# Kernel optimization log

Measured on AMD Instinct MI355X. Metric: run time of the kernel, lower is better.

Reference implementation:

```python
import jax, jax.numpy as jnp
import numpy as np

B_, H, N, D = 512, 8, 256, 16   # windows*batch, heads, tokens/window, head_dim
NW = 64                          # windows per image (B_ = 8 images * 64 windows)
TABLE = 961                      # (2*16-1)^2 relative position table rows
EPS = 1e-12                      # F.normalize eps


def setup_inputs() -> dict:
    key = jax.random.key(0)
    k_q, k_k, k_v, k_t, k_i, k_m = jax.random.split(key, 6)
    return {
        "q": jax.random.normal(k_q, (B_, H, N, D), dtype=jnp.float32),
        "k": jax.random.normal(k_k, (B_, H, N, D), dtype=jnp.float32),
        "v": jax.random.normal(k_v, (B_, H, N, D), dtype=jnp.float32),
        "table": jax.random.normal(k_t, (TABLE, H), dtype=jnp.float32),
        "index": jax.random.randint(k_i, (N * N,), 0, TABLE, dtype=jnp.int64),
        "mask": jax.random.normal(k_m, (NW, N, N), dtype=jnp.float32),
    }


def _l2norm(x):
    # matches F.normalize(x, dim=-1): x / max(||x||2, eps)
    n = jnp.sqrt(jnp.sum(x * x, axis=-1, keepdims=True))
    return x / jnp.maximum(n, EPS)


def reference(q, k, v, table, index, mask):
    b, h, n, d = q.shape
    # cosine-normalized QK^T: [B_, H, N, N]
    attn = jnp.einsum("bhnd,bhmd->bhnm", _l2norm(q), _l2norm(k))
    # relative position bias gather: table[index] -> (N*N, H) -> (H, N, N)
    bias = table[index].reshape(n, n, h).transpose(2, 0, 1)
    attn = attn + bias[None]
    # per-window additive mask
    nw = mask.shape[0]
    attn = attn.reshape(b // nw, nw, h, n, n) + mask[None, :, None]
    attn = attn.reshape(b, h, n, n)
    attn = jax.nn.softmax(attn, axis=-1)   # attn_drop is identity at p=0
    x = jnp.einsum("bhnm,bhmd->bhnd", attn, v)
    # transpose(1,2).reshape(B_, N, H*head_dim)
    return x.transpose(0, 2, 1, 3).reshape(b, n, h * d)
```

## Files before the change

### kernel.cpp

```cpp
#include <hip/hip_runtime.h>
#include <stdint.h>

#define HH 8
#define NN 256
#define DD 16
#define NWIN 64
#define LOG2E 1.44269504088896340736f

typedef __attribute__((ext_vector_type(8))) short short8;
typedef __attribute__((ext_vector_type(4))) short short4_t;
typedef __attribute__((ext_vector_type(4))) float f32x4;

static __device__ __forceinline__ unsigned short f2bf(float f) {
    union { float f; uint32_t u; } v; v.f = f;
    uint32_t u = v.u;
    uint32_t r = (u + 0x7fffu + ((u >> 16) & 1u)) >> 16;
    return (unsigned short)r;
}
static __device__ __forceinline__ float bf2f(uint32_t s) {
    union { uint32_t u; float f; } v; v.u = s << 16;
    return v.f;
}

__global__ void bias_perm_kernel(const float* __restrict__ table,
                                 const int* __restrict__ index,
                                 unsigned short* __restrict__ biasD) {
    int o = blockIdx.x * 256 + threadIdx.x;
    int r  = o & 3;
    int c  = (o >> 2) & 15;
    int qq = (o >> 6) & 3;
    int jt = (o >> 8) & 15;
    int it = (o >> 12) & 15;
    int h  = o >> 16;
    int i = it * 16 + c;
    int j = jt * 16 + qq * 4 + r;
    int idx = index[i * NN + j];
    biasD[o] = f2bf(table[idx * HH + h] * LOG2E);
}

__global__ void mask_perm_kernel(const float* __restrict__ mask,
                                 unsigned short* __restrict__ maskD) {
    __shared__ float lds[16 * 256];
    int w  = blockIdx.x >> 4;
    int it = blockIdx.x & 15;
    int tid = threadIdx.x;
    const float* src = mask + ((size_t)w * NN + it * 16) * NN;
    {
        int row = tid >> 4, col0 = (tid & 15) * 16;
        const float4* s4 = (const float4*)(src + row * NN + col0);
        float4* d4 = (float4*)(lds + row * 256 + col0);
        d4[0] = s4[0]; d4[1] = s4[1]; d4[2] = s4[2]; d4[3] = s4[3];
    }
    __syncthreads();
    unsigned short* dst = maskD + (size_t)blockIdx.x * 4096 + tid * 16;
    int base = tid * 16;
#pragma unroll
    for (int e = 0; e < 16; e++) {
        int o  = base + e;
        int r  = o & 3;
        int c  = (o >> 2) & 15;
        int qq = (o >> 6) & 3;
        int jt = (o >> 8) & 15;
        int j  = jt * 16 + qq * 4 + r;
        dst[e] = f2bf(lds[c * 256 + j] * LOG2E);
    }
}

__global__ __launch_bounds__(256, 2) void attn_kernel(
    const float* __restrict__ q, const float* __restrict__ k, const float* __restrict__ v,
    const unsigned short* __restrict__ biasD, const unsigned short* __restrict__ maskD,
    float* __restrict__ out)
{
    int bh = blockIdx.x;
    int b  = bh >> 3;
    int h  = bh & 7;
    int w  = b & (NWIN - 1);
    int tid  = threadIdx.x;
    int lane = tid & 63;
    int wave = tid >> 6;
    int c    = lane & 15;
    int quad = lane >> 4;

    __shared__ unsigned short Kn[256 * 20];
    __shared__ unsigned short Vl[4096];
    __shared__ float Xs[256 * 17];

    const size_t base = (size_t)bh * (NN * DD);

    {
        const float4* kr = (const float4*)(k + base + (size_t)tid * DD);
        float4 a0 = kr[0], a1 = kr[1], a2 = kr[2], a3 = kr[3];
        float x[16] = {a0.x,a0.y,a0.z,a0.w, a1.x,a1.y,a1.z,a1.w,
                       a2.x,a2.y,a2.z,a2.w, a3.x,a3.y,a3.z,a3.w};
        float ss = 0.f;
#pragma unroll
        for (int e = 0; e < 16; e++) ss += x[e] * x[e];
        float sc = 1.0f / fmaxf(sqrtf(ss), 1e-12f);
        unsigned short* dst = &Kn[tid * 20];
#pragma unroll
        for (int e = 0; e < 16; e++) dst[e] = f2bf(x[e] * sc);
    }
    {
        const float4* vr = (const float4*)(v + base + (size_t)tid * DD);
        float4 a0 = vr[0], a1 = vr[1], a2 = vr[2], a3 = vr[3];
        float x[16] = {a0.x,a0.y,a0.z,a0.w, a1.x,a1.y,a1.z,a1.w,
                       a2.x,a2.y,a2.z,a2.w, a3.x,a3.y,a3.z,a3.w};
        int j  = tid;
        int kc = j >> 5, hi = (j >> 4) & 1, qv = (j >> 2) & 3, r = j & 3;
        int jj = hi * 4 + r;
#pragma unroll
        for (int d = 0; d < 16; d++)
            Vl[((kc * 4 + qv) * 16 + d) * 8 + jj] = f2bf(x[d]);
    }
    __syncthreads();

    short8 vf[8];
#pragma unroll
    for (int kc = 0; kc < 8; kc++)
        vf[kc] = *(const short8*)&Vl[((kc * 4 + quad) * 16 + c) * 8];

    f32x4 zero = {0.f, 0.f, 0.f, 0.f};

#pragma unroll 1
    for (int t = 0; t < 4; t++) {
        int it = wave * 4 + t;
        int i0 = it * 16;

        short8 qf = {0,0,0,0,0,0,0,0};
        if (quad < 2) {
            const float4* qr = (const float4*)(q + base + (size_t)(i0 + c) * DD + quad * 8);
            float4 a0 = qr[0], a1 = qr[1];
            float x[8] = {a0.x,a0.y,a0.z,a0.w, a1.x,a1.y,a1.z,a1.w};
            float ss = 0.f;
#pragma unroll
            for (int e = 0; e < 8; e++) ss += x[e] * x[e];
            ss += __shfl_xor(ss, 16);
            float sc = LOG2E / fmaxf(sqrtf(ss), 1e-12f);
#pragma unroll
            for (int e = 0; e < 8; e++) qf[e] = (short)f2bf(x[e] * sc);
        }

        f32x4 acc[16];
#pragma unroll
        for (int jt = 0; jt < 16; jt++) {
            short8 kf = {0,0,0,0,0,0,0,0};
            if (quad < 2) {
                const unsigned short* kp = &Kn[(jt * 16 + c) * 20 + quad * 8];
                short4_t lo = *(const short4_t*)kp;
                short4_t hi = *(const short4_t*)(kp + 4);
                kf[0]=lo[0]; kf[1]=lo[1]; kf[2]=lo[2]; kf[3]=lo[3];
                kf[4]=hi[0]; kf[5]=hi[1]; kf[6]=hi[2]; kf[7]=hi[3];
            }
            acc[jt] = __builtin_amdgcn_mfma_f32_16x16x32_bf16(kf, qf, zero, 0, 0, 0);
        }

        const unsigned short* bD = biasD + (size_t)(h * 16 + it) * 4096 + quad * 64 + c * 4;
        const unsigned short* mD = maskD + (size_t)(w * 16 + it) * 4096 + quad * 64 + c * 4;
        float mx = -1e30f;
#pragma unroll
        for (int jt = 0; jt < 16; jt++) {
            uint2 bu = *(const uint2*)(bD + jt * 256);
            uint2 mu = *(const uint2*)(mD + jt * 256);
            acc[jt][0] += bf2f(bu.x & 0xffffu) + bf2f(mu.x & 0xffffu);
            acc[jt][1] += bf2f(bu.x >> 16)     + bf2f(mu.x >> 16);
            acc[jt][2] += bf2f(bu.y & 0xffffu) + bf2f(mu.y & 0xffffu);
            acc[jt][3] += bf2f(bu.y >> 16)     + bf2f(mu.y >> 16);
            mx = fmaxf(mx, fmaxf(fmaxf(acc[jt][0], acc[jt][1]),
                                 fmaxf(acc[jt][2], acc[jt][3])));
        }
        mx = fmaxf(mx, __shfl_xor(mx, 16));
        mx = fmaxf(mx, __shfl_xor(mx, 32));
        float sum = 0.f;
#pragma unroll
        for (int jt = 0; jt < 16; jt++) {
#pragma unroll
            for (int r = 0; r < 4; r++) {
                float e = __builtin_amdgcn_exp2f(acc[jt][r] - mx);
                acc[jt][r] = e;
                sum += e;
            }
        }
        sum += __shfl_xor(sum, 16);
        sum += __shfl_xor(sum, 32);
        float rs = __builtin_amdgcn_rcpf(sum);

        f32x4 xacc = {0.f, 0.f, 0.f, 0.f};
#pragma unroll
        for (int kc = 0; kc < 8; kc++) {
            short8 pf;
#pragma unroll
            for (int hi = 0; hi < 2; hi++) {
                int jt = kc * 2 + hi;
#pragma unroll
                for (int r = 0; r < 4; r++)
                    pf[hi * 4 + r] = (short)f2bf(acc[jt][r] * rs);
            }
            xacc = __builtin_amdgcn_mfma_f32_16x16x32_bf16(vf[kc], pf, xacc, 0, 0, 0);
        }

#pragma unroll
        for (int r = 0; r < 4; r++)
            Xs[(i0 + c) * 17 + quad * 4 + r] = xacc[r];
    }
    __syncthreads();

#pragma unroll
    for (int rep = 0; rep < 4; rep++) {
        int i    = rep * 64 + (tid >> 2);
        int part = tid & 3;
        float4 val;
        val.x = Xs[i * 17 + part * 4 + 0];
        val.y = Xs[i * 17 + part * 4 + 1];
        val.z = Xs[i * 17 + part * 4 + 2];
        val.w = Xs[i * 17 + part * 4 + 3];
        float4* dst = (float4*)(out + ((size_t)b * NN + i) * (HH * DD) + h * DD + part * 4);
        *dst = val;
    }
}

extern "C" void kernel_launch(void* const* d_in, const int* in_sizes, int n_in,
                              void* d_out, int out_size, void* d_ws, size_t ws_size,
                              hipStream_t stream) {
    const float* q     = (const float*)d_in[0];
    const float* k     = (const float*)d_in[1];
    const float* v     = (const float*)d_in[2];
    const float* table = (const float*)d_in[3];
    const int*   index = (const int*)d_in[4];
    const float* mask  = (const float*)d_in[5];
    float* out = (float*)d_out;

    unsigned short* biasD = (unsigned short*)d_ws;
    unsigned short* maskD = biasD + (size_t)HH * NN * NN;

    bias_perm_kernel<<<2048, 256, 0, stream>>>(table, index, biasD);
    mask_perm_kernel<<<1024, 256, 0, stream>>>(mask, maskD);
    attn_kernel<<<4096, 256, 0, stream>>>(q, k, v, biasD, maskD, out);
}
```

Before: 390.7 us.

## Drop softmax max pass, fold bias into MFMA accumulator, defer normalization

The bias and mask are loaded first and used as the initial MFMA accumulator, so the separate add pass goes away. The row-max reduction is replaced by a fixed offset of -16. This is exact in exact arithmetic, since cosine scores are bounded, but bias or mask values far above that offset could overflow exp2. Exponentials are packed straight into the PV MFMA, with a single reciprocal scale applied at output. Results are written directly to global memory instead of staging through LDS, and launch bounds are raised to 4 blocks per CU.

```diff
diff --git a/kernel.cpp b/kernel.cpp
--- a/kernel.cpp
+++ b/kernel.cpp
@@ -20,6 +20,10 @@
 static __device__ __forceinline__ float bf2f(uint32_t s) {
     union { uint32_t u; float f; } v; v.u = s << 16;
     return v.f;
+}
+static __device__ __forceinline__ uint32_t pack_bf16_rn(float a, float b) {
+    union { float f; uint32_t u; } x, y; x.f = a; y.f = b;
+    return __builtin_amdgcn_perm(y.u + 0x8000u, x.u + 0x8000u, 0x07060302u);
 }
 
 __global__ void bias_perm_kernel(const float* __restrict__ table,
@@ -66,7 +70,7 @@
     }
 }
 
-__global__ __launch_bounds__(256, 2) void attn_kernel(
+__global__ __launch_bounds__(256, 4) void attn_kernel(
     const float* __restrict__ q, const float* __restrict__ k, const float* __restrict__ v,
     const unsigned short* __restrict__ biasD, const unsigned short* __restrict__ maskD,
     float* __restrict__ out)
@@ -83,7 +87,6 @@
 
     __shared__ unsigned short Kn[256 * 20];
     __shared__ unsigned short Vl[4096];
-    __shared__ float Xs[256 * 17];
 
     const size_t base = (size_t)bh * (NN * DD);
 
@@ -119,8 +122,6 @@
     for (int kc = 0; kc < 8; kc++)
         vf[kc] = *(const short8*)&Vl[((kc * 4 + quad) * 16 + c) * 8];
 
-    f32x4 zero = {0.f, 0.f, 0.f, 0.f};
-
 #pragma unroll 1
     for (int t = 0; t < 4; t++) {
         int it = wave * 4 + t;
@@ -140,7 +141,19 @@
             for (int e = 0; e < 8; e++) qf[e] = (short)f2bf(x[e] * sc);
         }
 
+        const unsigned short* bD = biasD + (size_t)(h * 16 + it) * 4096 + quad * 64 + c * 4;
+        const unsigned short* mD = maskD + (size_t)(w * 16 + it) * 4096 + quad * 64 + c * 4;
         f32x4 acc[16];
+#pragma unroll
+        for (int jt = 0; jt < 16; jt++) {
+            uint2 bu = *(const uint2*)(bD + jt * 256);
+            uint2 mu = *(const uint2*)(mD + jt * 256);
+            acc[jt][0] = bf2f(bu.x & 0xffffu) + (bf2f(mu.x & 0xffffu) - 16.0f);
+            acc[jt][1] = bf2f(bu.x >> 16)     + (bf2f(mu.x >> 16)     - 16.0f);
+            acc[jt][2] = bf2f(bu.y & 0xffffu) + (bf2f(mu.y & 0xffffu) - 16.0f);
+            acc[jt][3] = bf2f(bu.y >> 16)     + (bf2f(mu.y >> 16)     - 16.0f);
+        }
+
 #pragma unroll
         for (int jt = 0; jt < 16; jt++) {
             short8 kf = {0,0,0,0,0,0,0,0};
@@ -151,69 +164,43 @@
                 kf[0]=lo[0]; kf[1]=lo[1]; kf[2]=lo[2]; kf[3]=lo[3];
                 kf[4]=hi[0]; kf[5]=hi[1]; kf[6]=hi[2]; kf[7]=hi[3];
             }
-            acc[jt] = __builtin_amdgcn_mfma_f32_16x16x32_bf16(kf, qf, zero, 0, 0, 0);
-        }
-
-        const unsigned short* bD = biasD + (size_t)(h * 16 + it) * 4096 + quad * 64 + c * 4;
-        const unsigned short* mD = maskD + (size_t)(w * 16 + it) * 4096 + quad * 64 + c * 4;
-        float mx = -1e30f;
-#pragma unroll
-        for (int jt = 0; jt < 16; jt++) {
-            uint2 bu = *(const uint2*)(bD + jt * 256);
-            uint2 mu = *(const uint2*)(mD + jt * 256);
-            acc[jt][0] += bf2f(bu.x & 0xffffu) + bf2f(mu.x & 0xffffu);
-            acc[jt][1] += bf2f(bu.x >> 16)     + bf2f(mu.x >> 16);
-            acc[jt][2] += bf2f(bu.y & 0xffffu) + bf2f(mu.y & 0xffffu);
-            acc[jt][3] += bf2f(bu.y >> 16)     + bf2f(mu.y >> 16);
-            mx = fmaxf(mx, fmaxf(fmaxf(acc[jt][0], acc[jt][1]),
-                                 fmaxf(acc[jt][2], acc[jt][3])));
-        }
-        mx = fmaxf(mx, __shfl_xor(mx, 16));
-        mx = fmaxf(mx, __shfl_xor(mx, 32));
-        float sum = 0.f;
-#pragma unroll
-        for (int jt = 0; jt < 16; jt++) {
-#pragma unroll
-            for (int r = 0; r < 4; r++) {
-                float e = __builtin_amdgcn_exp2f(acc[jt][r] - mx);
-                acc[jt][r] = e;
-                sum += e;
-            }
-        }
+            acc[jt] = __builtin_amdgcn_mfma_f32_16x16x32_bf16(kf, qf, acc[jt], 0, 0, 0);
+        }
+
+        float s0 = 0.f, s1 = 0.f, s2 = 0.f, s3 = 0.f;
+        f32x4 xacc = {0.f, 0.f, 0.f, 0.f};
+#pragma unroll
+        for (int kc = 0; kc < 8; kc++) {
+            float a0 = __builtin_amdgcn_exp2f(acc[kc * 2][0]);
+            float a1 = __builtin_amdgcn_exp2f(acc[kc * 2][1]);
+            float a2 = __builtin_amdgcn_exp2f(acc[kc * 2][2]);
+            float a3 = __builtin_amdgcn_exp2f(acc[kc * 2][3]);
+            float b0 = __builtin_amdgcn_exp2f(acc[kc * 2 + 1][0]);
+            float b1 = __builtin_amdgcn_exp2f(acc[kc * 2 + 1][1]);
+            float b2 = __builtin_amdgcn_exp2f(acc[kc * 2 + 1][2]);
+            float b3 = __builtin_amdgcn_exp2f(acc[kc * 2 + 1][3]);
+            s0 += a0 + b0;
+            s1 += a1 + b1;
+            s2 += a2 + b2;
+            s3 += a3 + b3;
+            union { short8 s8; uint32_t u[4]; } pp;
+            pp.u[0] = pack_bf16_rn(a0, a1);
+            pp.u[1] = pack_bf16_rn(a2, a3);
+            pp.u[2] = pack_bf16_rn(b0, b1);
+            pp.u[3] = pack_bf16_rn(b2, b3);
+            xacc = __builtin_amdgcn_mfma_f32_16x16x32_bf16(vf[kc], pp.s8, xacc, 0, 0, 0);
+        }
+        float sum = (s0 + s1) + (s2 + s3);
         sum += __shfl_xor(sum, 16);
         sum += __shfl_xor(sum, 32);
         float rs = __builtin_amdgcn_rcpf(sum);
 
-        f32x4 xacc = {0.f, 0.f, 0.f, 0.f};
-#pragma unroll
-        for (int kc = 0; kc < 8; kc++) {
-            short8 pf;
-#pragma unroll
-            for (int hi = 0; hi < 2; hi++) {
-                int jt = kc * 2 + hi;
-#pragma unroll
-                for (int r = 0; r < 4; r++)
-                    pf[hi * 4 + r] = (short)f2bf(acc[jt][r] * rs);
-            }
-            xacc = __builtin_amdgcn_mfma_f32_16x16x32_bf16(vf[kc], pf, xacc, 0, 0, 0);
-        }
-
-#pragma unroll
-        for (int r = 0; r < 4; r++)
-            Xs[(i0 + c) * 17 + quad * 4 + r] = xacc[r];
-    }
-    __syncthreads();
-
-#pragma unroll
-    for (int rep = 0; rep < 4; rep++) {
-        int i    = rep * 64 + (tid >> 2);
-        int part = tid & 3;
         float4 val;
-        val.x = Xs[i * 17 + part * 4 + 0];
-        val.y = Xs[i * 17 + part * 4 + 1];
-        val.z = Xs[i * 17 + part * 4 + 2];
-        val.w = Xs[i * 17 + part * 4 + 3];
-        float4* dst = (float4*)(out + ((size_t)b * NN + i) * (HH * DD) + h * DD + part * 4);
+        val.x = xacc[0] * rs;
+        val.y = xacc[1] * rs;
+        val.z = xacc[2] * rs;
+        val.w = xacc[3] * rs;
+        float4* dst = (float4*)(out + ((size_t)b * NN + (i0 + c)) * (HH * DD) + h * DD + quad * 4);
         *dst = val;
     }
 }
```

New measurement: 346.6 us. 1.13x faster.
